# Kernel tuning notes

Measured on AMD Instinct MI355X. Metric: run time of the kernel, lower is better.

Reference implementation:

```python
import jax, jax.numpy as jnp
import numpy as np


def _pe_2d(H, W, C, dtype):
    # PositionalEncodingPermute2D: returns (C, H, W)
    ch_half = (C + 1) // 2
    inv = 1.0 / (10000.0 ** (jnp.arange(0, ch_half, 2, dtype=jnp.float32) / ch_half))
    tH = jnp.arange(H, dtype=jnp.float32)
    tW = jnp.arange(W, dtype=jnp.float32)
    sinH = tH[:, None] * inv[None, :]              # (H, ch_half//2)
    sinW = tW[:, None] * inv[None, :]              # (W, ch_half//2)
    embH = jnp.concatenate([jnp.sin(sinH), jnp.cos(sinH)], axis=-1)  # (H, ch_half)
    embW = jnp.concatenate([jnp.sin(sinW), jnp.cos(sinW)], axis=-1)  # (W, ch_half)
    E = jnp.concatenate([
        jnp.broadcast_to(embW[None, :, :], (H, W, ch_half)),
        jnp.broadcast_to(embH[:, None, :], (H, W, ch_half)),
    ], axis=-1)[..., :C]                            # (H, W, C)
    return jnp.transpose(E, (2, 0, 1)).astype(dtype)  # (C, H, W)


def setup_inputs() -> dict:
    key = jax.random.key(0)
    k0, k1, k2, k3 = jax.random.split(key, 4)
    B, C, H, W = 4, 256, 64, 64
    s = 1.0 / np.sqrt(C)  # kaiming-ish scale
    return {
        "x": jax.random.normal(k0, (B, C, H, W), dtype=jnp.float32),
        "wq": jax.random.normal(k1, (C, C), dtype=jnp.float32) * s,
        "wk": jax.random.normal(k2, (C, C), dtype=jnp.float32) * s,
        "wv": jax.random.normal(k3, (C, C), dtype=jnp.float32) * s,
    }


def reference(x, wq, wk, wv):
    B, C, H, W = x.shape
    scale = C ** (-0.5)
    x = x + _pe_2d(H, W, C, x.dtype)[None]          # (B, C, H, W)
    X = x.reshape(B, C, H * W).transpose(0, 2, 1)   # (B, N, C)
    Q = jnp.einsum('bnc,dc->bnd', X, wq)
    K = jnp.einsum('bnc,dc->bnd', X, wk)
    V = jnp.einsum('bnc,dc->bnd', X, wv)
    A = jax.nn.softmax(jnp.einsum('bnd,bmd->bnm', Q, K) * scale, axis=-1)
    Y = jnp.einsum('bnm,bmd->bnd', A, V)            # (B, N, C)
    return Y.transpose(0, 2, 1).reshape(B, C, H, W)
```

## Files before the change

### kernel.cpp

```cpp
#include <hip/hip_runtime.h>
#include <hip/hip_bf16.h>

#define BB 4
#define CC 256
#define NN 4096
#define NSPLIT 4
#define KSPLIT (NN / NSPLIT)
#define NPAIR (KSPLIT / 64)

typedef __attribute__((ext_vector_type(8))) short short8;
typedef __attribute__((ext_vector_type(4))) float floatx4;
typedef __attribute__((ext_vector_type(4))) unsigned short ushortx4;

__device__ __forceinline__ float bf2f(unsigned short u) {
  union { unsigned int i; float f; } cv; cv.i = ((unsigned int)u) << 16; return cv.f;
}
__device__ __forceinline__ unsigned short f2bf(float f) {
  union { __hip_bfloat16 h; unsigned short u; } cv; cv.h = __float2bfloat16(f); return cv.u;
}

#define MFMA(a, b, c) __builtin_amdgcn_mfma_f32_16x16x32_bf16((a), (b), (c), 0, 0, 0)

__device__ __forceinline__ void dma16(const unsigned short* g, unsigned short* l) {
  __builtin_amdgcn_global_load_lds(
      (const __attribute__((address_space(1))) unsigned int*)g,
      (__attribute__((address_space(3))) unsigned int*)l, 16, 0, 0);
}
#define S_BARRIER __builtin_amdgcn_s_barrier()
#define MEMFENCE __asm__ volatile("" ::: "memory")

__global__ __launch_bounds__(256) void wcvt(const float* __restrict__ w0,
                                            const float* __restrict__ w1,
                                            const float* __restrict__ w2,
                                            unsigned short* __restrict__ o0,
                                            unsigned short* __restrict__ o1,
                                            unsigned short* __restrict__ o2) {
  const float* w = (blockIdx.y == 0) ? w0 : (blockIdx.y == 1) ? w1 : w2;
  unsigned short* o = (blockIdx.y == 0) ? o0 : (blockIdx.y == 1) ? o1 : o2;
  int i = (blockIdx.x * 256 + threadIdx.x) * 4;
  floatx4 v = *(const floatx4*)&w[i];
  ushortx4 p;
#pragma unroll
  for (int r = 0; r < 4; r++) p[r] = f2bf(v[r]);
  *(ushortx4*)&o[i] = p;
}

__global__ __launch_bounds__(256) void prep_x(const float* __restrict__ x,
                                              unsigned short* __restrict__ Xbf) {
  __shared__ float tile[32][33];
  int b = blockIdx.z;
  int n0 = blockIdx.x * 32, c0 = blockIdx.y * 32;
  int tx = threadIdx.x, ty = threadIdx.y;
#pragma unroll
  for (int i = 0; i < 4; i++) {
    int c = c0 + ty + i * 8;
    int n = n0 + tx;
    float v = x[((long)(b * CC + c)) * NN + n];
    int hh = n >> 6, ww = n & 63;
    int j = c & 63;
    float freq = exp2f(-0.2076205059304601f * (float)j);
    float arg = (float)((c < 128) ? ww : hh) * freq;
    v += (c & 64) ? cosf(arg) : sinf(arg);
    tile[ty + i * 8][tx] = v;
  }
  __syncthreads();
#pragma unroll
  for (int i = 0; i < 4; i++) {
    int n = n0 + ty + i * 8;
    int c = c0 + tx;
    Xbf[((long)(b * NN + n)) * CC + c] = f2bf(tile[tx][ty + i * 8]);
  }
}

__global__ __launch_bounds__(256, 2) void gemm_bt(const unsigned short* __restrict__ A, long asb,
                                                  const unsigned short* __restrict__ Bt, long bsb,
                                                  unsigned short* __restrict__ O, long osb,
                                                  int Nc) {
  __shared__ alignas(16) unsigned short Al[64][40];
  __shared__ alignas(16) unsigned short Bl[64][40];
  int b = blockIdx.z;
  const unsigned short* Ab = A + (long)b * asb;
  const unsigned short* Bb = Bt + (long)b * bsb;
  unsigned short* Ob = O + (long)b * osb;
  long row0 = (long)blockIdx.y * 64, col0 = (long)blockIdx.x * 64;
  int t = threadIdx.x, wave = t >> 6, lane = t & 63, quad = lane >> 4, l15 = lane & 15;
  int sr = t >> 2, sk = (t & 3) * 8;
  floatx4 acc[4] = {};
#pragma unroll
  for (int k0 = 0; k0 < 256; k0 += 32) {
    short8 av = *(const short8*)&Ab[(row0 + sr) * 256 + k0 + sk];
    short8 bv = *(const short8*)&Bb[(col0 + sr) * 256 + k0 + sk];
    __syncthreads();
    *(short8*)&Al[sr][sk] = av;
    *(short8*)&Bl[sr][sk] = bv;
    __syncthreads();
    short8 af = *(const short8*)&Al[wave * 16 + l15][quad * 8];
#pragma unroll
    for (int cb = 0; cb < 4; cb++) {
      short8 bf = *(const short8*)&Bl[cb * 16 + l15][quad * 8];
      acc[cb] = MFMA(af, bf, acc[cb]);
    }
  }
#pragma unroll
  for (int cb = 0; cb < 4; cb++) {
#pragma unroll
    for (int r = 0; r < 4; r++) {
      long row = row0 + wave * 16 + quad * 4 + r;
      long col = col0 + cb * 16 + l15;
      Ob[row * (long)Nc + col] = f2bf(acc[cb][r]);
    }
  }
}

__global__ __launch_bounds__(512, 1) void attn(const unsigned short* __restrict__ QKg,
                                               const unsigned short* __restrict__ Vtg,
                                               unsigned short* __restrict__ Opart,
                                               float* __restrict__ Lp) {
  __shared__ alignas(16) unsigned short Kl[4 * 8192];
  __shared__ alignas(16) unsigned short Vl[4 * 8192];
  __shared__ alignas(16) unsigned short Plf[8][2][512];
  int F = blockIdx.x;
  int c = F & 15, sp = c & 3, b = c >> 2;
  long q0 = (long)(F >> 4) * 256;
  int t = threadIdx.x, wave = t >> 6, lane = t & 63, quad = lane >> 4, l15 = lane & 15;
  const unsigned short* Qb = QKg + (long)b * NN * 512;
  const unsigned short* Kb = Qb + 256;
  const unsigned short* Vb = Vtg + (long)b * CC * NN;

  short8 qf[2][8];
#pragma unroll
  for (int qb = 0; qb < 2; qb++) {
    long qrow = q0 + wave * 32 + qb * 16 + l15;
#pragma unroll
    for (int ks = 0; ks < 8; ks++)
      qf[qb][ks] = *(const short8*)&Qb[qrow * 512 + ks * 32 + quad * 8];
  }

  floatx4 acc[2][17] = {};
  short8 ones;
#pragma unroll
  for (int j = 0; j < 8; j++) ones[j] = (short)0x3F80;

  const float sc = 0.0625f * 1.4426950408889634f;
  const int kbeg = sp * KSPLIT;

  auto stage_pair = [&](int p, int buf) {
#pragma unroll
    for (int tt = 0; tt < 2; tt++) {
      int m0 = kbeg + (p * 2 + tt) * 64 / 2;
      int slot = buf * 2 + tt;
#pragma unroll
      for (int st = 0; st < 2; st++) {
        int fg = st * 8 + wave;
        dma16(&Kb[(long)(m0 + st * 16 + l15) * 512 + wave * 32 + quad * 8],
              &Kl[slot * 8192 + fg * 512]);
        dma16(&Vb[(long)(fg * 16 + l15) * NN + m0 + quad * 8],
              &Vl[slot * 8192 + fg * 512]);
      }
    }
  };

  __builtin_amdgcn_s_waitcnt(0xF70);
  stage_pair(0, 0);
  MEMFENCE;

  for (int p = 0; p < NPAIR; p++) {
    int buf = p & 1;
    S_BARRIER;
    MEMFENCE;
    if (p + 1 < NPAIR) {
      stage_pair(p + 1, buf ^ 1);
      MEMFENCE;
      __builtin_amdgcn_s_waitcnt(0xF78);
    } else {
      __builtin_amdgcn_s_waitcnt(0xF70);
    }
    S_BARRIER;
    MEMFENCE;

#pragma unroll
    for (int tt = 0; tt < 2; tt++) {
      int kb = (buf * 2 + tt) * 8192;
      floatx4 s[2][2];
      {
        floatx4 z = {0.f, 0.f, 0.f, 0.f};
        s[0][0] = z; s[0][1] = z; s[1][0] = z; s[1][1] = z;
      }
#pragma unroll
      for (int fgk = 0; fgk < 16; fgk++) {
        short8 kf = *(const short8*)&Kl[kb + fgk * 512 + lane * 8];
        int mt = fgk >> 3, ks = fgk & 7;
        s[0][mt] = MFMA(qf[0][ks], kf, s[0][mt]);
        s[1][mt] = MFMA(qf[1][ks], kf, s[1][mt]);
      }

#pragma unroll
      for (int qb = 0; qb < 2; qb++) {
#pragma unroll
        for (int r = 0; r < 4; r++) {
          unsigned short pb0 = f2bf(__builtin_amdgcn_exp2f(s[qb][0][r] * sc));
          unsigned short pb1 = f2bf(__builtin_amdgcn_exp2f(s[qb][1][r] * sc));
          int m = quad * 4 + r;
          Plf[wave][qb][((l15 >> 3) * 16 + m) * 8 + (l15 & 7)] = pb0;
          Plf[wave][qb][((2 + (l15 >> 3)) * 16 + m) * 8 + (l15 & 7)] = pb1;
        }
      }
      MEMFENCE;
      short8 pf0 = *(const short8*)&Plf[wave][0][lane * 8];
      short8 pf1 = *(const short8*)&Plf[wave][1][lane * 8];
      acc[0][16] = MFMA(pf0, ones, acc[0][16]);
      acc[1][16] = MFMA(pf1, ones, acc[1][16]);
#pragma unroll
      for (int db = 0; db < 16; db++) {
        short8 vf = *(const short8*)&Vl[kb + db * 512 + lane * 8];
        acc[0][db] = MFMA(pf0, vf, acc[0][db]);
        acc[1][db] = MFMA(pf1, vf, acc[1][db]);
      }
      MEMFENCE;
    }
  }

  unsigned short* Ob = Opart + (long)(b * NSPLIT + sp) * CC * NN;
#pragma unroll
  for (int qb = 0; qb < 2; qb++) {
    long nidx = q0 + wave * 32 + qb * 16 + quad * 4;
#pragma unroll
    for (int db = 0; db < 16; db++) {
      long d = db * 16 + l15;
      ushortx4 pk;
#pragma unroll
      for (int r = 0; r < 4; r++) pk[r] = f2bf(acc[qb][db][r]);
      *(ushortx4*)&Ob[d * NN + nidx] = pk;
    }
    if (l15 == 0) {
#pragma unroll
      for (int r = 0; r < 4; r++)
        Lp[(long)(b * NSPLIT + sp) * NN + nidx + r] = acc[qb][16][r];
    }
  }
}

__global__ __launch_bounds__(256) void combine(const unsigned short* __restrict__ Op,
                                               const float* __restrict__ Lp,
                                               float* __restrict__ Out) {
  __shared__ float Wl[64];
  int b = blockIdx.z;
  int d0 = blockIdx.y * 64, n0 = blockIdx.x * 64;
  int t = threadIdx.x;
  if (t < 64) {
    int n = n0 + t;
    float L = 0.f;
#pragma unroll
    for (int s = 0; s < NSPLIT; s++) L += Lp[(long)(b * NSPLIT + s) * NN + n];
    Wl[t] = 1.0f / L;
  }
  __syncthreads();
  int tn = t & 15, td = t >> 4;
  int nb = n0 + tn * 4;
  float w[4];
#pragma unroll
  for (int r = 0; r < 4; r++) w[r] = Wl[tn * 4 + r];
#pragma unroll
  for (int dd = 0; dd < 4; dd++) {
    int d = d0 + td * 4 + dd;
    floatx4 o = {0.f, 0.f, 0.f, 0.f};
#pragma unroll
    for (int s = 0; s < NSPLIT; s++) {
      ushortx4 pv = *(const ushortx4*)&Op[((long)(b * NSPLIT + s) * CC + d) * NN + nb];
#pragma unroll
      for (int r = 0; r < 4; r++) o[r] += bf2f(pv[r]);
    }
#pragma unroll
    for (int r = 0; r < 4; r++) o[r] *= w[r];
    *(floatx4*)&Out[((long)b * CC + d) * NN + nb] = o;
  }
}

extern "C" void kernel_launch(void* const* d_in, const int* in_sizes, int n_in,
                              void* d_out, int out_size, void* d_ws, size_t ws_size,
                              hipStream_t stream) {
  const float* x = (const float*)d_in[0];
  const float* wq = (const float*)d_in[1];
  const float* wk = (const float*)d_in[2];
  const float* wv = (const float*)d_in[3];
  float* out = (float*)d_out;

  char* ws = (char*)d_ws;
  unsigned short* QKbuf = (unsigned short*)(ws);
  unsigned short* Vt = (unsigned short*)(ws + (16l << 20));
  unsigned short* Xbf = (unsigned short*)(ws + (24l << 20));
  unsigned short* Opart = (unsigned short*)(ws + (24l << 20));
  float* Lp = (float*)(ws + (56l << 20));
  unsigned short* Wqk = (unsigned short*)(ws + (57l << 20));
  unsigned short* Wv = (unsigned short*)(ws + (57l << 20) + (1 << 19));

  wcvt<<<dim3(CC * CC / 1024, 3), 256, 0, stream>>>(wq, wk, wv, Wqk, Wqk + CC * CC, Wv);
  prep_x<<<dim3(NN / 32, CC / 32, BB), dim3(32, 8), 0, stream>>>(x, Xbf);
  gemm_bt<<<dim3(512 / 64, NN / 64, BB), 256, 0, stream>>>(Xbf, (long)NN * CC, Wqk, 0, QKbuf,
                                                           (long)NN * 512, 512);
  gemm_bt<<<dim3(NN / 64, CC / 64, BB), 256, 0, stream>>>(Wv, 0, Xbf, (long)NN * CC, Vt,
                                                          (long)CC * NN, NN);
  attn<<<dim3(256), 512, 0, stream>>>(QKbuf, Vt, Opart, Lp);
  combine<<<dim3(NN / 64, CC / 64, BB), 256, 0, stream>>>(Opart, Lp, out);
}
```

Baseline: 201.0 us.

## Fuse QK and V projection GEMMs into one 128x128-tiled DMA double-buffered kernel

Replaces the two separate 64x64-tile projection GEMM launches with a single kernel whose block index selects either the QK or the V^T product. Each block now computes a 128x128 tile with a 4x4 MFMA grid per wave, which raises data reuse. Operands are staged through direct global-to-LDS loads with double buffering, so the next K slice loads while the current one computes. The cost is more accumulator registers per thread and fewer, larger blocks, which may reduce occupancy or leave the GPU less evenly loaded.

Result: faster. 194.1 us (-3.4%).

```diff
diff --git a/kernel.cpp b/kernel.cpp
--- a/kernel.cpp
+++ b/kernel.cpp
@@ -72,44 +72,88 @@
   }
 }
 
-__global__ __launch_bounds__(256, 2) void gemm_bt(const unsigned short* __restrict__ A, long asb,
-                                                  const unsigned short* __restrict__ Bt, long bsb,
-                                                  unsigned short* __restrict__ O, long osb,
-                                                  int Nc) {
-  __shared__ alignas(16) unsigned short Al[64][40];
-  __shared__ alignas(16) unsigned short Bl[64][40];
-  int b = blockIdx.z;
-  const unsigned short* Ab = A + (long)b * asb;
-  const unsigned short* Bb = Bt + (long)b * bsb;
-  unsigned short* Ob = O + (long)b * osb;
-  long row0 = (long)blockIdx.y * 64, col0 = (long)blockIdx.x * 64;
+__global__ __launch_bounds__(256, 2) void gemm_fused(const unsigned short* __restrict__ Xbf,
+                                                     const unsigned short* __restrict__ Wqk,
+                                                     const unsigned short* __restrict__ Wv,
+                                                     unsigned short* __restrict__ QK,
+                                                     unsigned short* __restrict__ Vt) {
+  __shared__ alignas(16) unsigned short Af[2][8 * 512];
+  __shared__ alignas(16) unsigned short Bf[2][8 * 512];
+  const unsigned short *Ab, *Bb;
+  unsigned short* Ob;
+  long row0, col0;
+  int ldo;
+  int F = blockIdx.x;
+  if (F < 512) {
+    int b = F >> 7, r = F & 127;
+    row0 = (long)(r >> 2) * 128;
+    col0 = (long)(r & 3) * 128;
+    Ab = Xbf + (long)b * NN * CC;
+    Bb = Wqk;
+    Ob = QK + (long)b * NN * 512;
+    ldo = 512;
+  } else {
+    int F2 = F - 512;
+    int b = F2 >> 6, r = F2 & 63;
+    row0 = (long)(r >> 5) * 128;
+    col0 = (long)(r & 31) * 128;
+    Ab = Wv;
+    Bb = Xbf + (long)b * NN * CC;
+    Ob = Vt + (long)b * CC * NN;
+    ldo = NN;
+  }
   int t = threadIdx.x, wave = t >> 6, lane = t & 63, quad = lane >> 4, l15 = lane & 15;
-  int sr = t >> 2, sk = (t & 3) * 8;
-  floatx4 acc[4] = {};
-#pragma unroll
-  for (int k0 = 0; k0 < 256; k0 += 32) {
-    short8 av = *(const short8*)&Ab[(row0 + sr) * 256 + k0 + sk];
-    short8 bv = *(const short8*)&Bb[(col0 + sr) * 256 + k0 + sk];
-    __syncthreads();
-    *(short8*)&Al[sr][sk] = av;
-    *(short8*)&Bl[sr][sk] = bv;
-    __syncthreads();
-    short8 af = *(const short8*)&Al[wave * 16 + l15][quad * 8];
-#pragma unroll
-    for (int cb = 0; cb < 4; cb++) {
-      short8 bf = *(const short8*)&Bl[cb * 16 + l15][quad * 8];
-      acc[cb] = MFMA(af, bf, acc[cb]);
-    }
-  }
-#pragma unroll
-  for (int cb = 0; cb < 4; cb++) {
-#pragma unroll
-    for (int r = 0; r < 4; r++) {
-      long row = row0 + wave * 16 + quad * 4 + r;
-      long col = col0 + cb * 16 + l15;
-      Ob[row * (long)Nc + col] = f2bf(acc[cb][r]);
-    }
-  }
+  int wr = wave >> 1, wc = wave & 1;
+
+  auto stage = [&](int k0, int buf) {
+#pragma unroll
+    for (int i = 0; i < 2; i++) {
+      int fg = wave * 2 + i;
+      dma16(&Ab[(row0 + fg * 16 + l15) * 256 + k0 + quad * 8], &Af[buf][fg * 512]);
+      dma16(&Bb[(col0 + fg * 16 + l15) * 256 + k0 + quad * 8], &Bf[buf][fg * 512]);
+    }
+  };
+
+  floatx4 acc[4][4] = {};
+  stage(0, 0);
+  MEMFENCE;
+#pragma unroll
+  for (int ki = 0; ki < 8; ki++) {
+    int buf = ki & 1;
+    S_BARRIER;
+    MEMFENCE;
+    if (ki + 1 < 8) {
+      stage((ki + 1) * 32, buf ^ 1);
+      MEMFENCE;
+      __builtin_amdgcn_s_waitcnt(0xF74);
+    } else {
+      __builtin_amdgcn_s_waitcnt(0xF70);
+    }
+    S_BARRIER;
+    MEMFENCE;
+    short8 af[4], bf[4];
+#pragma unroll
+    for (int i = 0; i < 4; i++) {
+      af[i] = *(const short8*)&Af[buf][(wr * 4 + i) * 512 + lane * 8];
+      bf[i] = *(const short8*)&Bf[buf][(wc * 4 + i) * 512 + lane * 8];
+    }
+#pragma unroll
+    for (int i = 0; i < 4; i++)
+#pragma unroll
+      for (int j = 0; j < 4; j++) acc[i][j] = MFMA(af[i], bf[j], acc[i][j]);
+  }
+
+#pragma unroll
+  for (int i = 0; i < 4; i++)
+#pragma unroll
+    for (int j = 0; j < 4; j++) {
+      long col = col0 + (wc * 4 + j) * 16 + l15;
+#pragma unroll
+      for (int r = 0; r < 4; r++) {
+        long row = row0 + (wr * 4 + i) * 16 + quad * 4 + r;
+        Ob[row * (long)ldo + col] = f2bf(acc[i][j][r]);
+      }
+    }
 }
 
 __global__ __launch_bounds__(512, 1) void attn(const unsigned short* __restrict__ QKg,
@@ -147,7 +191,7 @@
   auto stage_pair = [&](int p, int buf) {
 #pragma unroll
     for (int tt = 0; tt < 2; tt++) {
-      int m0 = kbeg + (p * 2 + tt) * 64 / 2;
+      int m0 = kbeg + (p * 2 + tt) * 32;
       int slot = buf * 2 + tt;
 #pragma unroll
       for (int st = 0; st < 2; st++) {
@@ -296,10 +340,7 @@
 
   wcvt<<<dim3(CC * CC / 1024, 3), 256, 0, stream>>>(wq, wk, wv, Wqk, Wqk + CC * CC, Wv);
   prep_x<<<dim3(NN / 32, CC / 32, BB), dim3(32, 8), 0, stream>>>(x, Xbf);
-  gemm_bt<<<dim3(512 / 64, NN / 64, BB), 256, 0, stream>>>(Xbf, (long)NN * CC, Wqk, 0, QKbuf,
-                                                           (long)NN * 512, 512);
-  gemm_bt<<<dim3(NN / 64, CC / 64, BB), 256, 0, stream>>>(Wv, 0, Xbf, (long)NN * CC, Vt,
-                                                          (long)CC * NN, NN);
+  gemm_fused<<<dim3(768), 256, 0, stream>>>(Xbf, Wqk, Wv, QKbuf, Vt);
   attn<<<dim3(256), 512, 0, stream>>>(QKbuf, Vt, Opart, Lp);
   combine<<<dim3(NN / 64, CC / 64, BB), 256, 0, stream>>>(Opart, Lp, out);
 }
```
